# Optimization experiments

Hardware: AMD Instinct MI355X
Metric: run time of the kernel (lower is better)

The kernel has to match this reference:

```python
import jax, jax.numpy as jnp
import numpy as np

B, T, D = 2, 1024, 1024
H, DK = 16, 64  # n_head, d_k; inner dim = H*DK = D
INV_SQRT_DK = 1.0 / float(np.sqrt(DK))


def setup_inputs() -> dict:
    key = jax.random.key(0)
    ks = jax.random.split(key, 16)
    init = lambda k, shape: (jax.random.normal(k, shape, dtype=jnp.float32) * 0.02)
    return {
        "query": jax.random.normal(ks[0], (B, T, D), dtype=jnp.float32),
        "key": jax.random.normal(ks[1], (B, T, D), dtype=jnp.float32),
        "value": jax.random.normal(ks[2], (B, T, D), dtype=jnp.float32),
        "pos_k": jax.random.normal(ks[3], (T, T, DK), dtype=jnp.float32),
        "pos_v": jax.random.normal(ks[4], (T, T, DK), dtype=jnp.float32),
        "mask": jnp.ones((B, T, T), dtype=jnp.int32),
        "relative_attention_bias": jax.random.normal(ks[5], (1, H, T, T), dtype=jnp.float32),
        "Wq": init(ks[6], (D, D)), "bq": init(ks[7], (D,)),
        "Wk": init(ks[8], (D, D)), "bk": init(ks[9], (D,)),
        "Wv": init(ks[10], (D, D)), "bv": init(ks[11], (D,)),
        "Wo": init(ks[12], (D, D)), "bo": init(ks[13], (D,)),
    }


def reference(query, key, value, pos_k, pos_v, mask, relative_attention_bias,
              Wq, bq, Wk, bk, Wv, bv, Wo, bo):
    nb = query.shape[0]
    # projections -> (B, H, T, DK); q pre-scaled by 1/sqrt(d_k)
    q = (query @ Wq + bq).reshape(nb, -1, H, DK).transpose(0, 2, 1, 3) * INV_SQRT_DK
    k = (key @ Wk + bk).reshape(nb, -1, H, DK).transpose(0, 2, 1, 3)
    v = (value @ Wv + bv).reshape(nb, -1, H, DK).transpose(0, 2, 1, 3)

    # content scores + relative-position key scores (B, H, T, S)
    A = jnp.einsum('bhtd,bhsd->bhts', q, k)
    Bp = jnp.einsum('bhtd,tsd->bhts', q, pos_k)
    scores = A + Bp + relative_attention_bias

    # masked softmax: mask (B, T, S) -> invalid where mask == 0
    inv = (mask[:, None, :, :] == 0)  # (B, 1, T, S)
    scores = jnp.where(inv, -jnp.inf, scores)
    attn = jax.nn.softmax(scores, axis=-1)
    attn = jnp.where(inv, 0.0, attn)

    # value aggregation + relative-position value term
    x = jnp.einsum('bhts,bhsd->bhtd', attn, v)
    x = x + jnp.einsum('bhts,tsd->bhtd', attn, pos_v)

    x = x.transpose(0, 2, 1, 3).reshape(nb, -1, H * DK)  # (B, T, D)
    return x @ Wo + bo
```

## Files before the change

### kernel.cpp

```cpp
#include <hip/hip_runtime.h>


#define DEV __device__ __forceinline__

typedef short bf16x8 __attribute__((ext_vector_type(8)));
typedef float f32x4 __attribute__((ext_vector_type(4)));

DEV short f2b(float f) {
  unsigned u = __builtin_bit_cast(unsigned, f);
  u = (u + 0x7FFFu + ((u >> 16) & 1u)) >> 16;
  return (short)u;
}
DEV float b2f(short s) {
  unsigned u = ((unsigned)(unsigned short)s) << 16;
  return __builtin_bit_cast(float, u);
}

#define MFMA(a, b, c) __builtin_amdgcn_mfma_f32_16x16x32_bf16(a, b, c, 0, 0, 0)

DEV void gload16(const void* g, void* l) {
  __builtin_amdgcn_global_load_lds(
      (const __attribute__((address_space(1))) void*)g,
      (__attribute__((address_space(3))) void*)l, 16, 0, 0);
}

__global__ __launch_bounds__(256) void k_cvt3(
    const float* __restrict__ a, const float* __restrict__ b, const float* __restrict__ c,
    short* __restrict__ oa, short* __restrict__ ob, short* __restrict__ oc) {
  const float* src = blockIdx.y == 0 ? a : (blockIdx.y == 1 ? b : c);
  short* dst = blockIdx.y == 0 ? oa : (blockIdx.y == 1 ? ob : oc);
  size_t i = ((size_t)blockIdx.x * 256 + threadIdx.x) * 8;
  float4 p0 = *(const float4*)(src + i);
  float4 p1 = *(const float4*)(src + i + 4);
  bf16x8 o;
  o[0] = f2b(p0.x); o[1] = f2b(p0.y); o[2] = f2b(p0.z); o[3] = f2b(p0.w);
  o[4] = f2b(p1.x); o[5] = f2b(p1.y); o[6] = f2b(p1.z); o[7] = f2b(p1.w);
  *(bf16x8*)(dst + i) = o;
}

__global__ __launch_bounds__(256) void k_wtrans4(
    const float* __restrict__ w0, const float* __restrict__ w1,
    const float* __restrict__ w2, const float* __restrict__ w3,
    short* __restrict__ o0, short* __restrict__ o1,
    short* __restrict__ o2, short* __restrict__ o3) {
  const float* src; short* dst;
  switch (blockIdx.z) {
    case 0: src = w0; dst = o0; break;
    case 1: src = w1; dst = o1; break;
    case 2: src = w2; dst = o2; break;
    default: src = w3; dst = o3;
  }
  __shared__ short LW[64][74];
  const int tid = threadIdx.x;
  const int k0 = blockIdx.y * 64, n0 = blockIdx.x * 64;
  {
    int c4 = (tid & 15) * 4;
#pragma unroll
    for (int i = 0; i < 4; ++i) {
      int r = (tid >> 4) + i * 16;
      float4 v = *(const float4*)(src + (size_t)(k0 + r) * 1024 + n0 + c4);
      LW[r][c4 + 0] = f2b(v.x); LW[r][c4 + 1] = f2b(v.y);
      LW[r][c4 + 2] = f2b(v.z); LW[r][c4 + 3] = f2b(v.w);
    }
  }
  __syncthreads();
  {
    int n = tid >> 2, kb = (tid & 3) * 16;
#pragma unroll
    for (int j2 = 0; j2 < 2; ++j2) {
      int kk = kb + j2 * 8;
      bf16x8 o;
#pragma unroll
      for (int j = 0; j < 8; ++j) o[j] = LW[kk + j][n];
      *(bf16x8*)(dst + (size_t)(n0 + n) * 1024 + k0 + kk) = o;
    }
  }
}

__global__ __launch_bounds__(256) void k_qkv(
    const short* __restrict__ Ain, const short* __restrict__ WT,
    const float* __restrict__ bq, const float* __restrict__ bk,
    const float* __restrict__ bv,
    short* __restrict__ qo, short* __restrict__ ko, short* __restrict__ vTo) {
  __shared__ short As[128 * 32];
  __shared__ short Bs[64 * 32];
  __shared__ short LW[128][72];
  const int tid = threadIdx.x;
  const int w = tid >> 6, l = tid & 63, lg = l >> 4, lr = l & 15;
  const int wm = w >> 1, wn = w & 1;
  const int n0 = blockIdx.x * 64;
  const int m0 = blockIdx.y * 128;
  const int seg = m0 >> 11;
  const int mseg = m0 & 2047;
  const short* Abase = Ain + ((size_t)m0 << 10);
  const short* Bbase = WT + ((size_t)seg << 20) + ((size_t)n0 << 10);
  const int srow = l >> 2, scol8 = (l & 3) * 8;
  f32x4 acc[4][2] = {};
  for (int k0 = 0; k0 < 1024; k0 += 32) {
    gload16(Abase + (size_t)((w * 2) * 16 + srow) * 1024 + k0 + scol8, &As[(w * 2) * 512]);
    gload16(Abase + (size_t)((w * 2 + 1) * 16 + srow) * 1024 + k0 + scol8, &As[(w * 2 + 1) * 512]);
    gload16(Bbase + (size_t)(w * 16 + srow) * 1024 + k0 + scol8, &Bs[w * 512]);
    __syncthreads();
    bf16x8 af[4], bf[2];
#pragma unroll
    for (int i = 0; i < 4; ++i) af[i] = *(const bf16x8*)&As[(wm * 64 + i * 16 + lr) * 32 + lg * 8];
#pragma unroll
    for (int i = 0; i < 2; ++i) bf[i] = *(const bf16x8*)&Bs[(wn * 32 + i * 16 + lr) * 32 + lg * 8];
#pragma unroll
    for (int mi = 0; mi < 4; ++mi)
#pragma unroll
      for (int ni = 0; ni < 2; ++ni) acc[mi][ni] = MFMA(af[mi], bf[ni], acc[mi][ni]);
    __syncthreads();
  }
  const float* bias = seg == 0 ? bq : (seg == 1 ? bk : bv);
  const float scale = seg == 0 ? 0.125f : 1.0f;
  float bvals[2];
#pragma unroll
  for (int ni = 0; ni < 2; ++ni) bvals[ni] = bias[n0 + wn * 32 + ni * 16 + lr];
#pragma unroll
  for (int mi = 0; mi < 4; ++mi)
#pragma unroll
    for (int ni = 0; ni < 2; ++ni)
#pragma unroll
      for (int r = 0; r < 4; ++r)
        LW[wm * 64 + mi * 16 + lg * 4 + r][wn * 32 + ni * 16 + lr] =
            f2b((acc[mi][ni][r] + bvals[ni]) * scale);
  __syncthreads();
  if (seg < 2) {
    short* dst = seg == 0 ? qo : ko;
    int r = tid >> 1, half = tid & 1;
    int m = mseg + r, b = m >> 10, t = m & 1023;
    int h = n0 >> 6;
#pragma unroll
    for (int g = 0; g < 4; ++g) {
      int dk = half * 32 + g * 8;
      bf16x8 o = *(const bf16x8*)&LW[r][dk];
      *(bf16x8*)(dst + (((size_t)(b * 16 + h) * 1024 + t) << 6) + dk) = o;
    }
  } else {
    int dkc = tid & 63, th = tid >> 6;
    int h = n0 >> 6, dk = dkc;
    int b = mseg >> 10;
    int tbase = (mseg & 1023) + th * 32;
#pragma unroll
    for (int g = 0; g < 4; ++g) {
      bf16x8 o;
#pragma unroll
      for (int e = 0; e < 8; ++e) o[e] = LW[th * 32 + g * 8 + e][dkc];
      *(bf16x8*)(vTo + (((size_t)(b * 16 + h) * 64 + dk) << 10) + tbase + g * 8) = o;
    }
  }
}

__global__ __launch_bounds__(512, 2) void k_qk(
    const short* __restrict__ q, const short* __restrict__ kmat,
    short* __restrict__ S) {
  const int bh = blockIdx.y;
  const int tid = threadIdx.x;
  const int w = tid >> 6, l = tid & 63, lg = l >> 4, lr = l & 15;
  const int wm = w >> 2, wn = w & 3;
  const int t0 = blockIdx.x * 32 + wm * 16;
  const int scol = wn * 256;
  __shared__ short LS[8][16][266];

  bf16x8 af[2];
#pragma unroll
  for (int kk = 0; kk < 2; ++kk)
    af[kk] = *(const bf16x8*)(q + ((size_t)bh * 1024 + (t0 + lr)) * 64 + kk * 32 + lg * 8);

#pragma unroll
  for (int ni = 0; ni < 16; ++ni) {
    int s = scol + ni * 16 + lr;
    const short* kp = kmat + ((size_t)bh * 1024 + s) * 64 + lg * 8;
    f32x4 a = {};
    a = MFMA(af[0], *(const bf16x8*)kp, a);
    a = MFMA(af[1], *(const bf16x8*)(kp + 32), a);
#pragma unroll
    for (int r = 0; r < 4; ++r) LS[w][lg * 4 + r][ni * 16 + lr] = f2b(a[r]);
  }
  short* sb = S + ((size_t)bh * 1024 + t0) * 1024 + scol;
  const int r2 = l >> 5, c16 = (l & 31) * 8;
#pragma unroll
  for (int rr = 0; rr < 8; ++rr) {
    int row = rr * 2 + r2;
    bf16x8 o = *(const bf16x8*)&LS[w][row][c16];
    *(bf16x8*)(sb + (size_t)row * 1024 + c16) = o;
  }
}

__global__ __launch_bounds__(256) void k_posk_exp(
    const short* __restrict__ q, const float* __restrict__ pos_k,
    const float* __restrict__ rab, const int* __restrict__ mask,
    short* __restrict__ S) {
  const int t = blockIdx.y;
  const int tid = threadIdx.x;
  const int w = tid >> 6, l = tid & 63, lg = l >> 4, lr = l & 15;
  const int sB = blockIdx.x * 256;
  const int s0 = sB + w * 64;
  __shared__ float RB[16][260];
  __shared__ int MK[2][260];
  __shared__ short SW[4][32][66];
  {
    int hr = tid >> 4, c0 = (tid & 15) * 4;
#pragma unroll
    for (int it = 0; it < 4; ++it) {
      int c = c0 + it * 64;
      float4 v = *(const float4*)(rab + ((size_t)hr * 1024 + t) * 1024 + sB + c);
      RB[hr][c] = v.x; RB[hr][c + 1] = v.y; RB[hr][c + 2] = v.z; RB[hr][c + 3] = v.w;
    }
  }
  if (tid < 128) {
    int br = tid >> 6, c = (tid & 63) * 4;
    int4 mv = *(const int4*)(mask + ((size_t)br * 1024 + t) * 1024 + sB + c);
    MK[br][c] = mv.x; MK[br][c + 1] = mv.y; MK[br][c + 2] = mv.z; MK[br][c + 3] = mv.w;
  }
  {
#pragma unroll
    for (int rr = 0; rr < 4; ++rr) {
      int row = (l >> 3) + rr * 8;
      int s8 = (l & 7) * 8;
      *(bf16x8*)&SW[w][row][s8] =
          *(const bf16x8*)(S + ((size_t)row * 1024 + t) * 1024 + s0 + s8);
    }
  }
  bf16x8 af[2][2];
#pragma unroll
  for (int mi = 0; mi < 2; ++mi)
#pragma unroll
    for (int kk = 0; kk < 2; ++kk) {
      int bh = mi * 16 + lr;
      af[mi][kk] = *(const bf16x8*)(q + ((size_t)bh * 1024 + t) * 64 + kk * 32 + lg * 8);
    }
  f32x4 acc[2][4] = {};
#pragma unroll
  for (int ni = 0; ni < 4; ++ni) {
    int s = s0 + ni * 16 + lr;
#pragma unroll
    for (int kk = 0; kk < 2; ++kk) {
      const float* pk = pos_k + ((size_t)t * 1024 + s) * 64 + kk * 32 + lg * 8;
      const float4 p0 = *(const float4*)pk;
      const float4 p1 = *(const float4*)(pk + 4);
      bf16x8 bfr;
      bfr[0] = f2b(p0.x); bfr[1] = f2b(p0.y); bfr[2] = f2b(p0.z); bfr[3] = f2b(p0.w);
      bfr[4] = f2b(p1.x); bfr[5] = f2b(p1.y); bfr[6] = f2b(p1.z); bfr[7] = f2b(p1.w);
#pragma unroll
      for (int mi = 0; mi < 2; ++mi) acc[mi][ni] = MFMA(af[mi][kk], bfr, acc[mi][ni]);
    }
  }
  __syncthreads();
#pragma unroll
  for (int ni = 0; ni < 4; ++ni) {
    int colw = w * 64 + ni * 16 + lr;
    int col = ni * 16 + lr;
    int msk0 = MK[0][colw];
    int msk1 = MK[1][colw];
#pragma unroll
    for (int r = 0; r < 4; ++r) {
      int h = lg * 4 + r;
      float bv = RB[h][colw];
      float v0 = acc[0][ni][r] + bv + b2f(SW[w][h][col]);
      float v1 = acc[1][ni][r] + bv + b2f(SW[w][16 + h][col]);
      float e0 = (msk0 == 0) ? 0.f : __expf(v0 - 10.f);
      float e1 = (msk1 == 0) ? 0.f : __expf(v1 - 10.f);
      SW[w][h][col] = f2b(e0);
      SW[w][16 + h][col] = f2b(e1);
    }
  }
#pragma unroll
  for (int rr = 0; rr < 4; ++rr) {
    int row = (l >> 3) + rr * 8;
    int s8 = (l & 7) * 8;
    bf16x8 o = *(const bf16x8*)&SW[w][row][s8];
    *(bf16x8*)(S + ((size_t)row * 1024 + t) * 1024 + s0 + s8) = o;
  }
}

__global__ __launch_bounds__(256) void k_posv(
    const short* __restrict__ S, const float* __restrict__ pos_v,
    short* __restrict__ X0h) {
  const int t = blockIdx.x;
  const int tid = threadIdx.x;
  const int w = tid >> 6, l = tid & 63, lg = l >> 4, lr = l & 15;
  const int mi = w >> 1;
  const int nb = (w & 1) * 2;
  __shared__ short pv[256][66];
  f32x4 acc[2] = {};
  const int srow = tid >> 4;
  const int dk4 = (tid & 15) * 4;
  for (int c = 0; c < 4; ++c) {
    int sc = c * 256;
    if (c) __syncthreads();
#pragma unroll
    for (int it = 0; it < 16; ++it) {
      int s = srow + it * 16;
      float4 p = *(const float4*)(pos_v + ((size_t)t * 1024 + sc + s) * 64 + dk4);
      unsigned p0 = (unsigned)(unsigned short)f2b(p.x) | ((unsigned)(unsigned short)f2b(p.y) << 16);
      unsigned p1 = (unsigned)(unsigned short)f2b(p.z) | ((unsigned)(unsigned short)f2b(p.w) << 16);
      *(unsigned*)&pv[s][dk4] = p0;
      *(unsigned*)&pv[s][dk4 + 2] = p1;
    }
    __syncthreads();
    const int bh = mi * 16 + lr;
#pragma unroll
    for (int kk = 0; kk < 8; ++kk) {
      bf16x8 afr = *(const bf16x8*)(S + ((size_t)bh * 1024 + t) * 1024 + sc + kk * 32 + lg * 8);
#pragma unroll
      for (int ni = 0; ni < 2; ++ni) {
        int dk = (nb + ni) * 16 + lr;
        bf16x8 bfr;
#pragma unroll
        for (int j = 0; j < 8; ++j) bfr[j] = pv[kk * 32 + lg * 8 + j][dk];
        acc[ni] = MFMA(afr, bfr, acc[ni]);
      }
    }
  }
#pragma unroll
  for (int ni = 0; ni < 2; ++ni)
#pragma unroll
    for (int r = 0; r < 4; ++r) {
      int bh = mi * 16 + lg * 4 + r;
      int b = bh >> 4, h = bh & 15;
      int dk = (nb + ni) * 16 + lr;
      X0h[((size_t)(b * 1024 + t)) * 1024 + h * 64 + dk] = f2b(acc[ni][r]);
    }
}

__global__ __launch_bounds__(256) void k_av(
    const short* __restrict__ S, const short* __restrict__ vT,
    const short* __restrict__ X0h, short* __restrict__ X) {
  const int bh = blockIdx.y;
  const int tt0 = blockIdx.x * 32;
  const int tid = threadIdx.x;
  const int w = tid >> 6, l = tid & 63, lg = l >> 4, lr = l & 15;
  const int wm = w >> 1, wn = w & 1;
  const short* vbase = vT + ((size_t)bh << 16) + ((size_t)(wn * 32) << 10);
  const short* sbase = S + ((size_t)bh << 20) + ((size_t)(tt0 + wm * 16) << 10);
  f32x4 acc[2] = {};
  float lsum = 0.f;
#pragma unroll 8
  for (int kk = 0; kk < 32; ++kk) {
    bf16x8 afr = *(const bf16x8*)(sbase + ((size_t)lr << 10) + kk * 32 + lg * 8);
#pragma unroll
    for (int j = 0; j < 8; ++j) lsum += b2f(afr[j]);
#pragma unroll
    for (int ni = 0; ni < 2; ++ni) {
      bf16x8 bfr = *(const bf16x8*)(vbase + ((size_t)(ni * 16 + lr) << 10) + kk * 32 + lg * 8);
      acc[ni] = MFMA(afr, bfr, acc[ni]);
    }
  }
  lsum += __shfl_xor(lsum, 16);
  lsum += __shfl_xor(lsum, 32);
  const int b = bh >> 4, h = bh & 15;
#pragma unroll
  for (int ni = 0; ni < 2; ++ni)
#pragma unroll
    for (int r = 0; r < 4; ++r) {
      float lrow = __shfl(lsum, lg * 4 + r);
      float inv = 1.0f / lrow;
      int tt = tt0 + wm * 16 + lg * 4 + r;
      int d = h * 64 + wn * 32 + ni * 16 + lr;
      size_t idx = ((size_t)(b * 1024 + tt)) * 1024 + d;
      X[idx] = f2b((b2f(X0h[idx]) + acc[ni][r]) * inv);
    }
}

__global__ __launch_bounds__(256) void k_oproj(
    const short* __restrict__ X, const short* __restrict__ WT,
    const float* __restrict__ bias, float* __restrict__ out) {
  __shared__ short As[64 * 32];
  __shared__ short Bs[64 * 32];
  const int tid = threadIdx.x;
  const int w = tid >> 6, l = tid & 63, lg = l >> 4, lr = l & 15;
  const int wm = w >> 1, wn = w & 1;
  const int n0 = blockIdx.x * 64;
  const int m0 = blockIdx.y * 64;
  const short* Abase = X + ((size_t)m0 << 10);
  const short* Bbase = WT + ((size_t)n0 << 10);
  const int srow = l >> 2, scol8 = (l & 3) * 8;
  f32x4 acc[2][2] = {};
  for (int k0 = 0; k0 < 1024; k0 += 32) {
    gload16(Abase + (size_t)(w * 16 + srow) * 1024 + k0 + scol8, &As[w * 512]);
    gload16(Bbase + (size_t)(w * 16 + srow) * 1024 + k0 + scol8, &Bs[w * 512]);
    __syncthreads();
    bf16x8 af[2], bf[2];
#pragma unroll
    for (int i = 0; i < 2; ++i) af[i] = *(const bf16x8*)&As[(wm * 32 + i * 16 + lr) * 32 + lg * 8];
#pragma unroll
    for (int i = 0; i < 2; ++i) bf[i] = *(const bf16x8*)&Bs[(wn * 32 + i * 16 + lr) * 32 + lg * 8];
#pragma unroll
    for (int mi = 0; mi < 2; ++mi)
#pragma unroll
      for (int ni = 0; ni < 2; ++ni) acc[mi][ni] = MFMA(af[mi], bf[ni], acc[mi][ni]);
    __syncthreads();
  }
  float bvals[2];
#pragma unroll
  for (int ni = 0; ni < 2; ++ni) bvals[ni] = bias[n0 + wn * 32 + ni * 16 + lr];
#pragma unroll
  for (int mi = 0; mi < 2; ++mi)
#pragma unroll
    for (int ni = 0; ni < 2; ++ni)
#pragma unroll
      for (int r = 0; r < 4; ++r) {
        int m = m0 + wm * 32 + mi * 16 + lg * 4 + r;
        int n = n0 + wn * 32 + ni * 16 + lr;
        out[(size_t)m * 1024 + n] = acc[mi][ni][r] + bvals[ni];
      }
}

extern "C" void kernel_launch(void* const* d_in, const int* in_sizes, int n_in,
                              void* d_out, int out_size, void* d_ws, size_t ws_size,
                              hipStream_t stream) {
  (void)in_sizes; (void)n_in; (void)out_size; (void)ws_size;
  const float* query = (const float*)d_in[0];
  const float* key   = (const float*)d_in[1];
  const float* value = (const float*)d_in[2];
  const float* pos_k = (const float*)d_in[3];
  const float* pos_v = (const float*)d_in[4];
  const int*   mask  = (const int*)d_in[5];
  const float* rab   = (const float*)d_in[6];
  const float* Wq = (const float*)d_in[7];
  const float* bq = (const float*)d_in[8];
  const float* Wk = (const float*)d_in[9];
  const float* bk = (const float*)d_in[10];
  const float* Wv = (const float*)d_in[11];
  const float* bv = (const float*)d_in[12];
  const float* Wo = (const float*)d_in[13];
  const float* bo = (const float*)d_in[14];
  float* out = (float*)d_out;

  const size_t M2 = 2ull * 1024 * 1024;
  short* q   = (short*)d_ws;
  short* k   = q + M2;
  short* vT  = k + M2;
  short* S   = vT + M2;
  short* X0h = S + 32ull * 1024 * 1024;
  short* X   = X0h + M2;
  short* qin = X + M2;
  short* kin = qin + M2;
  short* vin = kin + M2;
  short* WqT = vin + M2;
  short* WkT = WqT + 1024 * 1024;
  short* WvT = WkT + 1024 * 1024;
  short* WoT = WvT + 1024 * 1024;

  k_cvt3<<<dim3(1024, 3), dim3(256), 0, stream>>>(query, key, value, qin, kin, vin);
  k_wtrans4<<<dim3(16, 16, 4), dim3(256), 0, stream>>>(Wq, Wk, Wv, Wo, WqT, WkT, WvT, WoT);
  k_qkv<<<dim3(16, 48), dim3(256), 0, stream>>>(qin, WqT, bq, bk, bv, q, k, vT);
  k_qk<<<dim3(32, 32), dim3(512), 0, stream>>>(q, k, S);
  k_posk_exp<<<dim3(4, 1024), dim3(256), 0, stream>>>(q, pos_k, rab, mask, S);
  k_posv<<<dim3(1024), dim3(256), 0, stream>>>(S, pos_v, X0h);
  k_av<<<dim3(32, 32), dim3(256), 0, stream>>>(S, vT, X0h, X);
  k_oproj<<<dim3(16, 32), dim3(256), 0, stream>>>(X, WoT, bo, out);
}
```

Measured before the change: 309.7 us.

## Split pos_v aggregation over two S halves, transpose pos_v tile in LDS, swizzle qkv grid

k_posv now launches two blocks per query row, each covering half of the key dimension. The two partial results go to separate buffers, and k_av sums them while adding the rest of its output. The pos_v tile is stored transposed in LDS so each B fragment is read with two 4-wide loads instead of eight strided scalar loads. k_qkv also remaps block indices with an XCD-style swizzle. The split doubles the partial-output traffic and adds one extra read in k_av, in exchange for more parallelism and fewer LDS read instructions.

```diff
diff --git a/kernel.cpp b/kernel.cpp
--- a/kernel.cpp
+++ b/kernel.cpp
@@ -4,6 +4,7 @@
 #define DEV __device__ __forceinline__
 
 typedef short bf16x8 __attribute__((ext_vector_type(8)));
+typedef short bf16x4 __attribute__((ext_vector_type(4)));
 typedef float f32x4 __attribute__((ext_vector_type(4)));
 
 DEV short f2b(float f) {
@@ -88,8 +89,10 @@
   const int tid = threadIdx.x;
   const int w = tid >> 6, l = tid & 63, lg = l >> 4, lr = l & 15;
   const int wm = w >> 1, wn = w & 1;
-  const int n0 = blockIdx.x * 64;
-  const int m0 = blockIdx.y * 128;
+  const int flat = blockIdx.x + gridDim.x * blockIdx.y;
+  const int flat2 = (flat & 7) * 96 + (flat >> 3);
+  const int n0 = (flat2 & 15) * 64;
+  const int m0 = (flat2 >> 4) * 128;
   const int seg = m0 >> 11;
   const int mseg = m0 & 2047;
   const short* Abase = Ain + ((size_t)m0 << 10);
@@ -277,39 +280,51 @@
 
 __global__ __launch_bounds__(256) void k_posv(
     const short* __restrict__ S, const float* __restrict__ pos_v,
-    short* __restrict__ X0h) {
-  const int t = blockIdx.x;
+    short* __restrict__ X0p) {
+  const int half = blockIdx.x;
+  const int t = blockIdx.y;
   const int tid = threadIdx.x;
   const int w = tid >> 6, l = tid & 63, lg = l >> 4, lr = l & 15;
   const int mi = w >> 1;
   const int nb = (w & 1) * 2;
-  __shared__ short pv[256][66];
+  __shared__ short pvT[64][132];
   f32x4 acc[2] = {};
-  const int srow = tid >> 4;
+  const int spair = tid >> 4;
   const int dk4 = (tid & 15) * 4;
+  const int sbase = half * 512;
   for (int c = 0; c < 4; ++c) {
-    int sc = c * 256;
+    const int sc = sbase + c * 128;
     if (c) __syncthreads();
 #pragma unroll
-    for (int it = 0; it < 16; ++it) {
-      int s = srow + it * 16;
-      float4 p = *(const float4*)(pos_v + ((size_t)t * 1024 + sc + s) * 64 + dk4);
-      unsigned p0 = (unsigned)(unsigned short)f2b(p.x) | ((unsigned)(unsigned short)f2b(p.y) << 16);
-      unsigned p1 = (unsigned)(unsigned short)f2b(p.z) | ((unsigned)(unsigned short)f2b(p.w) << 16);
-      *(unsigned*)&pv[s][dk4] = p0;
-      *(unsigned*)&pv[s][dk4 + 2] = p1;
+    for (int it = 0; it < 4; ++it) {
+      int srel = spair * 2 + it * 32;
+      const float* p0 = pos_v + ((size_t)t * 1024 + sc + srel) * 64 + dk4;
+      float4 a = *(const float4*)p0;
+      float4 b = *(const float4*)(p0 + 64);
+      unsigned u0 = (unsigned)(unsigned short)f2b(a.x) | ((unsigned)(unsigned short)f2b(b.x) << 16);
+      unsigned u1 = (unsigned)(unsigned short)f2b(a.y) | ((unsigned)(unsigned short)f2b(b.y) << 16);
+      unsigned u2 = (unsigned)(unsigned short)f2b(a.z) | ((unsigned)(unsigned short)f2b(b.z) << 16);
+      unsigned u3 = (unsigned)(unsigned short)f2b(a.w) | ((unsigned)(unsigned short)f2b(b.w) << 16);
+      *(unsigned*)&pvT[dk4 + 0][srel] = u0;
+      *(unsigned*)&pvT[dk4 + 1][srel] = u1;
+      *(unsigned*)&pvT[dk4 + 2][srel] = u2;
+      *(unsigned*)&pvT[dk4 + 3][srel] = u3;
     }
     __syncthreads();
     const int bh = mi * 16 + lr;
-#pragma unroll
-    for (int kk = 0; kk < 8; ++kk) {
-      bf16x8 afr = *(const bf16x8*)(S + ((size_t)bh * 1024 + t) * 1024 + sc + kk * 32 + lg * 8);
+    const short* sBp = S + ((size_t)bh * 1024 + t) * 1024 + sc;
+#pragma unroll
+    for (int kk = 0; kk < 4; ++kk) {
+      bf16x8 afr = *(const bf16x8*)(sBp + kk * 32 + lg * 8);
 #pragma unroll
       for (int ni = 0; ni < 2; ++ni) {
         int dk = (nb + ni) * 16 + lr;
+        const short* pp = &pvT[dk][kk * 32 + lg * 8];
+        bf16x4 lo = *(const bf16x4*)pp;
+        bf16x4 hi = *(const bf16x4*)(pp + 4);
         bf16x8 bfr;
-#pragma unroll
-        for (int j = 0; j < 8; ++j) bfr[j] = pv[kk * 32 + lg * 8 + j][dk];
+        bfr[0] = lo[0]; bfr[1] = lo[1]; bfr[2] = lo[2]; bfr[3] = lo[3];
+        bfr[4] = hi[0]; bfr[5] = hi[1]; bfr[6] = hi[2]; bfr[7] = hi[3];
         acc[ni] = MFMA(afr, bfr, acc[ni]);
       }
     }
@@ -318,16 +333,17 @@
   for (int ni = 0; ni < 2; ++ni)
 #pragma unroll
     for (int r = 0; r < 4; ++r) {
-      int bh = mi * 16 + lg * 4 + r;
-      int b = bh >> 4, h = bh & 15;
+      int bh2 = mi * 16 + lg * 4 + r;
+      int b = bh2 >> 4, h = bh2 & 15;
       int dk = (nb + ni) * 16 + lr;
-      X0h[((size_t)(b * 1024 + t)) * 1024 + h * 64 + dk] = f2b(acc[ni][r]);
+      X0p[((size_t)half << 21) + ((size_t)(b * 1024 + t)) * 1024 + h * 64 + dk] =
+          f2b(acc[ni][r]);
     }
 }
 
 __global__ __launch_bounds__(256) void k_av(
     const short* __restrict__ S, const short* __restrict__ vT,
-    const short* __restrict__ X0h, short* __restrict__ X) {
+    const short* __restrict__ X0p, short* __restrict__ X) {
   const int bh = blockIdx.y;
   const int tt0 = blockIdx.x * 32;
   const int tid = threadIdx.x;
@@ -360,7 +376,7 @@
       int tt = tt0 + wm * 16 + lg * 4 + r;
       int d = h * 64 + wn * 32 + ni * 16 + lr;
       size_t idx = ((size_t)(b * 1024 + tt)) * 1024 + d;
-      X[idx] = f2b((b2f(X0h[idx]) + acc[ni][r]) * inv);
+      X[idx] = f2b((b2f(X0p[idx]) + b2f(X0p[idx + (1u << 21)]) + acc[ni][r]) * inv);
     }
 }
 
@@ -434,8 +450,8 @@
   short* k   = q + M2;
   short* vT  = k + M2;
   short* S   = vT + M2;
-  short* X0h = S + 32ull * 1024 * 1024;
-  short* X   = X0h + M2;
+  short* X0p = S + 32ull * 1024 * 1024;
+  short* X   = X0p + 2 * M2;
   short* qin = X + M2;
   short* kin = qin + M2;
   short* vin = kin + M2;
@@ -449,7 +465,7 @@
   k_qkv<<<dim3(16, 48), dim3(256), 0, stream>>>(qin, WqT, bq, bk, bv, q, k, vT);
   k_qk<<<dim3(32, 32), dim3(512), 0, stream>>>(q, k, S);
   k_posk_exp<<<dim3(4, 1024), dim3(256), 0, stream>>>(q, pos_k, rab, mask, S);
-  k_posv<<<dim3(1024), dim3(256), 0, stream>>>(S, pos_v, X0h);
-  k_av<<<dim3(32, 32), dim3(256), 0, stream>>>(S, vT, X0h, X);
+  k_posv<<<dim3(2, 1024), dim3(256), 0, stream>>>(S, pos_v, X0p);
+  k_av<<<dim3(32, 32), dim3(256), 0, stream>>>(S, vT, X0p, X);
   k_oproj<<<dim3(16, 32), dim3(256), 0, stream>>>(X, WoT, bo, out);
 }
```

New measurement: 311.7 us. About the same (+0.6%).
